# Performance work log

Measured on AMD Instinct MI355X. Metric: run time of the kernel, lower is better.

## Reference

```python
import jax, jax.numpy as jnp
import numpy as np

B, S, H = 32, 64, 512
ATT = 128


def _window_index_tables(seq_len):
    # Enumerate all contiguous windows of size 2..S, same set (order-independent
    # for the softmax-weighted sum) as the torch double loop.
    starts, ends = [], []
    for w in range(2, seq_len + 1):
        for s in range(0, seq_len - w + 1):
            starts.append(s)
            ends.append(s + w)
    starts = np.asarray(starts, np.int32)
    ends = np.asarray(ends, np.int32)
    widths = ends - starts
    ks = np.floor(np.log2(widths)).astype(np.int32)  # sparse-table level per window
    e2 = ends - (1 << ks)                            # second gather position
    return starts, e2, ks


def setup_inputs() -> dict:
    key = jax.random.key(0)
    k0, k1, k2, k3, k4 = jax.random.split(key, 5)
    return {
        "lstm_out": jax.random.normal(k0, (B, S, H), dtype=jnp.float32),
        "W1": jax.random.normal(k1, (H, ATT), dtype=jnp.float32) * 0.05,
        "b1": jax.random.normal(k2, (ATT,), dtype=jnp.float32) * 0.05,
        "W2": jax.random.normal(k3, (ATT, 1), dtype=jnp.float32) * 0.05,
        "b2": jax.random.normal(k4, (1,), dtype=jnp.float32) * 0.05,
    }


def reference(lstm_out, W1, b1, W2, b2):
    b, s, h = lstm_out.shape
    # Sparse table: M[k][:, i] = max over lstm_out[:, i : i+2^k] (clipped to s).
    n_levels = int(np.floor(np.log2(s))) + 1
    tables = [lstm_out]
    for k in range(1, n_levels):
        half = 1 << (k - 1)
        prev = tables[-1]
        shifted = jnp.concatenate(
            [prev[:, half:], jnp.full((b, half, h), -jnp.inf, prev.dtype)], axis=1)
        tables.append(jnp.maximum(prev, shifted))
    Mstack = jnp.stack(tables)  # [K, B, S, H]

    starts, e2, ks = _window_index_tables(s)
    # Range max of each window = max of two overlapping power-of-two blocks.
    pooled = jnp.maximum(Mstack[ks, :, starts], Mstack[ks, :, e2])  # [n_win, B, H]
    pooled = jnp.transpose(pooled, (1, 0, 2))  # [B, n_win, H]

    hid = jax.nn.relu(jnp.einsum("bnh,ha->bna", pooled, W1) + b1)
    scores = jnp.einsum("bna,ao->bno", hid, W2) + b2  # [B, n_win, 1]
    attn = jax.nn.softmax(scores, axis=1)
    return jnp.sum(attn * pooled, axis=1)  # [B, H]
```

## Files before the change

### kernel.cpp

```cpp
#include <hip/hip_runtime.h>
#include <stdint.h>


typedef unsigned short u16;
typedef unsigned int u32;

#define B_    32
#define S_    64
#define H_    512
#define ATT_  128
#define NWIN  2016
#define NLEV  7
#define TLEV  6

typedef __bf16 bf16x8 __attribute__((ext_vector_type(8)));
typedef float  f32x4  __attribute__((ext_vector_type(4)));

__device__ __forceinline__ float asf(u32 i) {
  union { u32 i; float f; } v; v.i = i; return v.f;
}
__device__ __forceinline__ u32 asu(float f) {
  union { float f; u32 i; } v; v.f = f; return v.i;
}
__device__ __forceinline__ float bf2f(u16 u) { return asf(((u32)u) << 16); }
__device__ __forceinline__ u16 f2bf(float f) {
  u32 i = asu(f);
  i += 0x7fffu + ((i >> 16) & 1u);
  return (u16)(i >> 16);
}
__device__ __forceinline__ u32 bfmax2(u32 a, u32 b) {
  float a0 = asf(a << 16), a1 = asf(a & 0xffff0000u);
  float b0 = asf(b << 16), b1 = asf(b & 0xffff0000u);
  u32 m0 = asu(fmaxf(a0, b0)), m1 = asu(fmaxf(a1, b1));
  return (m1 & 0xffff0000u) | (m0 >> 16);
}
__device__ __forceinline__ uint4 bfmax8(uint4 a, uint4 b) {
  uint4 m;
  m.x = bfmax2(a.x, b.x); m.y = bfmax2(a.y, b.y);
  m.z = bfmax2(a.z, b.z); m.w = bfmax2(a.w, b.w);
  return m;
}
__device__ __forceinline__ bf16x8 as_bf16x8(uint4 v) {
  union { uint4 u; bf16x8 h; } c; c.u = v; return c.h;
}

__launch_bounds__(256)
__global__ void k01_init(const float* __restrict__ lstm, const float* __restrict__ W1,
                         u16* __restrict__ table, u16* __restrict__ w1t,
                         u16* __restrict__ widx) {
  int bid = blockIdx.x, tid = threadIdx.x;
  __shared__ u16 bufA[64 * 64], bufB[64 * 64];

  {
    int idx = bid * 256 + tid;
    int n = idx >> 9, kq = idx & 511;
    w1t[idx] = f2bf(W1[kq * ATT_ + n]);
  }
  if (bid < 8) {
    int n = bid * 256 + tid;
    if (n < NWIN) {
      int w = 2, rem = n;
      while (rem >= 65 - w) { rem -= 65 - w; ++w; }
      int s = rem;
      int k = 31 - __clz(w);
      int e2 = s + w - (1 << k);
      widx[n] = (u16)(s | (e2 << 6) | (k << 12));
    }
  }

  int hc = bid & 7, b = bid >> 3;
  const float* src = lstm + (size_t)b * S_ * H_ + hc * 64;
  u16* tb = table + (size_t)b * TLEV * S_ * H_ + hc * 64;
  for (int t = tid; t < 64 * 16; t += 256) {
    int r = t >> 4, c4 = t & 15;
    float4 f = *reinterpret_cast<const float4*>(src + r * H_ + c4 * 4);
    ushort4 u;
    u.x = f2bf(f.x); u.y = f2bf(f.y); u.z = f2bf(f.z); u.w = f2bf(f.w);
    *reinterpret_cast<ushort4*>(&bufA[r * 64 + c4 * 4]) = u;
  }
  u16* pa = bufA; u16* pb = bufB;
  for (int k = 1; k < NLEV; ++k) {
    __syncthreads();
    int half = 1 << (k - 1);
    u16* dst_g = tb + (size_t)(k - 1) * S_ * H_;
    for (int t = tid; t < 64 * 16; t += 256) {
      int r = t >> 4, c4 = t & 15;
      int r2 = r + half; if (r2 > 63) r2 = 63;
      uint2 a  = *reinterpret_cast<const uint2*>(&pa[r  * 64 + c4 * 4]);
      uint2 bq = *reinterpret_cast<const uint2*>(&pa[r2 * 64 + c4 * 4]);
      uint2 m; m.x = bfmax2(a.x, bq.x); m.y = bfmax2(a.y, bq.y);
      *reinterpret_cast<uint2*>(&pb[r * 64 + c4 * 4]) = m;
      *reinterpret_cast<uint2*>(dst_g + r * H_ + c4 * 4) = m;
    }
    u16* tmp = pa; pa = pb; pb = tmp;
  }
}

__launch_bounds__(256, 1)
__global__ void k2_scores(const u16* __restrict__ table, const u16* __restrict__ w1t,
                          const float* __restrict__ b1, const float* __restrict__ w2,
                          const u16* __restrict__ widx, float* __restrict__ scores) {
  const int b = blockIdx.y, mt = blockIdx.x;
  __shared__ u16 Ts[2][128 * 64];
  __shared__ u16 Bs[2][128 * 64];
  __shared__ u16 widx_l[256];
  __shared__ float b1s[128], w2s[128];
  int tid = threadIdx.x;
  {
    int n = mt * 256 + tid; if (n > NWIN - 1) n = NWIN - 1;
    widx_l[tid] = widx[n];
  }
  if (tid < 128) { b1s[tid] = b1[tid]; w2s[tid] = w2[tid]; }
  __syncthreads();

  const int lv_lo = widx_l[0] >> 12;
  const u16* tb = table + (size_t)b * TLEV * S_ * H_ + (size_t)(lv_lo - 1) * S_ * H_;

  const u16* gT[4]; const u16* gB[4]; int sl[4];
#pragma unroll
  for (int p = 0; p < 4; ++p) {
    int slot = p * 256 + tid;
    int r = slot >> 3, c = slot & 7;
    int csw = (c ^ (r & 7)) * 8;
    gT[p] = tb  + r * H_ + csw;
    gB[p] = w1t + r * H_ + csw;
    sl[p] = slot * 8;
  }

#define DMA(KC, BSEL) do {                                                     \
    int ko_ = (KC) * 64;                                                       \
    _Pragma("unroll")                                                          \
    for (int p_ = 0; p_ < 4; ++p_) {                                           \
      __builtin_amdgcn_global_load_lds(                                        \
          (const __attribute__((address_space(1))) void*)(gT[p_] + ko_),       \
          (__attribute__((address_space(3))) void*)(&Ts[(BSEL)][sl[p_]]),      \
          16, 0, 0);                                                           \
      __builtin_amdgcn_global_load_lds(                                        \
          (const __attribute__((address_space(1))) void*)(gB[p_] + ko_),       \
          (__attribute__((address_space(3))) void*)(&Bs[(BSEL)][sl[p_]]),      \
          16, 0, 0);                                                           \
    }                                                                          \
  } while (0)

  int wid = tid >> 6, lane = tid & 63;
  int lrow = lane & 15, quad = lane >> 4;

  int aoff[4][2][2];
#pragma unroll
  for (int mi = 0; mi < 4; ++mi) {
    int pk = widx_l[wid * 64 + mi * 16 + lrow];
    int s = pk & 63, e2 = (pk >> 6) & 63, lv = (pk >> 12) - lv_lo;
    int rs = lv * 64 + s, re = lv * 64 + e2;
#pragma unroll
    for (int k2i = 0; k2i < 2; ++k2i) {
      int c = quad + k2i * 4;
      aoff[mi][k2i][0] = rs * 64 + ((c ^ (rs & 7)) * 8);
      aoff[mi][k2i][1] = re * 64 + ((c ^ (re & 7)) * 8);
    }
  }
  int boff[8][2];
#pragma unroll
  for (int j = 0; j < 8; ++j) {
    int n = j * 16 + lrow;
#pragma unroll
    for (int k2i = 0; k2i < 2; ++k2i) {
      int c = quad + k2i * 4;
      boff[j][k2i] = n * 64 + ((c ^ (n & 7)) * 8);
    }
  }

  f32x4 acc[4][8];
#pragma unroll
  for (int mi = 0; mi < 4; ++mi)
#pragma unroll
    for (int j = 0; j < 8; ++j) acc[mi][j] = (f32x4){0.f, 0.f, 0.f, 0.f};

  DMA(0, 0);

  for (int kc = 0; kc < 8; ++kc) {
    __syncthreads();
    if (kc < 7) DMA(kc + 1, (kc + 1) & 1);
    const u16* Tc = Ts[kc & 1];
    const u16* Bc = Bs[kc & 1];
#pragma unroll
    for (int k2i = 0; k2i < 2; ++k2i) {
      bf16x8 bfr[8];
#pragma unroll
      for (int j = 0; j < 8; ++j)
        bfr[j] = *reinterpret_cast<const bf16x8*>(&Bc[boff[j][k2i]]);
#pragma unroll
      for (int mi = 0; mi < 4; ++mi) {
        uint4 va = *reinterpret_cast<const uint4*>(&Tc[aoff[mi][k2i][0]]);
        uint4 vb = *reinterpret_cast<const uint4*>(&Tc[aoff[mi][k2i][1]]);
        bf16x8 af = as_bf16x8(bfmax8(va, vb));
#pragma unroll
        for (int j = 0; j < 8; ++j)
          acc[mi][j] = __builtin_amdgcn_mfma_f32_16x16x32_bf16(af, bfr[j], acc[mi][j], 0, 0, 0);
      }
    }
  }
#undef DMA

#pragma unroll
  for (int mi = 0; mi < 4; ++mi) {
#pragma unroll
    for (int r = 0; r < 4; ++r) {
      float p = 0.f;
#pragma unroll
      for (int j = 0; j < 8; ++j) {
        int n = j * 16 + lrow;
        float v = acc[mi][j][r] + b1s[n];
        p += (v > 0.f ? v : 0.f) * w2s[n];
      }
      p += __shfl_xor(p, 1, 16);
      p += __shfl_xor(p, 2, 16);
      p += __shfl_xor(p, 4, 16);
      p += __shfl_xor(p, 8, 16);
      if (lrow == 0) {
        int nw = mt * 256 + wid * 64 + mi * 16 + quad * 4 + r;
        if (nw < NWIN) scores[b * NWIN + nw] = p;
      }
    }
  }
}

__launch_bounds__(256)
__global__ void k34_out(const u16* __restrict__ table, const float* __restrict__ scores,
                        const u16* __restrict__ widx, float* __restrict__ out) {
  int hc = blockIdx.x, b = blockIdx.y, tid = threadIdx.x;
  __shared__ u16 Tl[TLEV * 64 * 64];
  __shared__ float attn_l[NWIN];
  __shared__ u16 widx_l[NWIN];
  __shared__ float red[4][64];
  __shared__ float wredM[4], wredS[4];
  const u16* tb = table + (size_t)b * TLEV * S_ * H_;
  int h0 = hc * 64;
  int lane = tid & 63, wid = tid >> 6;

  for (int t = tid; t < TLEV * 64 * 8; t += 256) {
    int row = t >> 3, c = t & 7;
    uint4 v = *reinterpret_cast<const uint4*>(tb + row * H_ + h0 + c * 8);
    *reinterpret_cast<uint4*>(&Tl[row * 64 + ((c ^ (row & 7)) * 8)]) = v;
  }
  for (int n = tid; n < NWIN; n += 256) widx_l[n] = widx[n];

  float mx = -1e30f;
  for (int n = tid; n < NWIN; n += 256) {
    float v = scores[b * NWIN + n];
    attn_l[n] = v;
    mx = fmaxf(mx, v);
  }
#pragma unroll
  for (int off = 32; off > 0; off >>= 1) mx = fmaxf(mx, __shfl_xor(mx, off, 64));
  if (lane == 0) wredM[wid] = mx;
  __syncthreads();
  mx = fmaxf(fmaxf(wredM[0], wredM[1]), fmaxf(wredM[2], wredM[3]));
  float sum = 0.f;
  for (int n = tid; n < NWIN; n += 256) {
    float e = __expf(attn_l[n] - mx);
    attn_l[n] = e;
    sum += e;
  }
#pragma unroll
  for (int off = 32; off > 0; off >>= 1) sum += __shfl_xor(sum, off, 64);
  if (lane == 0) wredS[wid] = sum;
  __syncthreads();
  float inv = 1.f / (wredS[0] + wredS[1] + wredS[2] + wredS[3]);

  int hq = tid & 7, g = tid >> 3;
  float acc[8];
#pragma unroll
  for (int j = 0; j < 8; ++j) acc[j] = 0.f;
  for (int i = 0; i < 63; ++i) {
    int n = g * 63 + i;
    int pk = widx_l[n];
    float a = attn_l[n];
    int s = pk & 63, e2 = (pk >> 6) & 63, lv = pk >> 12;
    int rs = (lv - 1) * 64 + s, re = (lv - 1) * 64 + e2;
    uint4 va = *reinterpret_cast<const uint4*>(&Tl[rs * 64 + ((hq ^ (rs & 7)) * 8)]);
    uint4 vb = *reinterpret_cast<const uint4*>(&Tl[re * 64 + ((hq ^ (re & 7)) * 8)]);
    u32 ua, ub;
#define ACC2(UA, UB, J0) do {                                            \
      float xa0 = asf((UA) << 16), xa1 = asf((UA) & 0xffff0000u);        \
      float xb0 = asf((UB) << 16), xb1 = asf((UB) & 0xffff0000u);        \
      acc[(J0)]     = fmaf(a, fmaxf(xa0, xb0), acc[(J0)]);               \
      acc[(J0) + 1] = fmaf(a, fmaxf(xa1, xb1), acc[(J0) + 1]);           \
    } while (0)
    ua = va.x; ub = vb.x; ACC2(ua, ub, 0);
    ua = va.y; ub = vb.y; ACC2(ua, ub, 2);
    ua = va.z; ub = vb.z; ACC2(ua, ub, 4);
    ua = va.w; ub = vb.w; ACC2(ua, ub, 6);
#undef ACC2
  }

#pragma unroll
  for (int j = 0; j < 8; ++j) {
    acc[j] += __shfl_xor(acc[j], 8, 64);
    acc[j] += __shfl_xor(acc[j], 16, 64);
    acc[j] += __shfl_xor(acc[j], 32, 64);
  }
  if (lane < 8) {
#pragma unroll
    for (int j = 0; j < 8; ++j) red[wid][hq * 8 + j] = acc[j];
  }
  __syncthreads();
  if (tid < 64) {
    float s2 = red[0][tid] + red[1][tid] + red[2][tid] + red[3][tid];
    out[b * H_ + h0 + tid] = s2 * inv;
  }
}

extern "C" void kernel_launch(void* const* d_in, const int* in_sizes, int n_in,
                              void* d_out, int out_size, void* d_ws, size_t ws_size,
                              hipStream_t stream) {
  const float* lstm = (const float*)d_in[0];
  const float* W1   = (const float*)d_in[1];
  const float* b1   = (const float*)d_in[2];
  const float* W2   = (const float*)d_in[3];
  float* out = (float*)d_out;

  char* ws = (char*)d_ws;
  u16*   widx   = (u16*)(ws + 0);
  u16*   w1t    = (u16*)(ws + 4096);
  u16*   table  = (u16*)(ws + 135168);
  float* scores = (float*)(ws + 12718080);

  k01_init <<<256, 256, 0, stream>>>(lstm, W1, table, w1t, widx);
  k2_scores<<<dim3(8, B_), 256, 0, stream>>>(table, w1t, b1, W2, widx, scores);
  k34_out  <<<dim3(8, B_), 256, 0, stream>>>(table, scores, widx, out);
}
```

Before: 116.0 us.

## Fuse three kernels into one cooperative kernel with grid syncs and LDS-resident tables

```diff
diff --git a/kernel.cpp b/kernel.cpp
--- a/kernel.cpp
+++ b/kernel.cpp
@@ -1,6 +1,9 @@
 #include <hip/hip_runtime.h>
+#include <hip/hip_cooperative_groups.h>
 #include <stdint.h>
 
+
+namespace cg = cooperative_groups;
 
 typedef unsigned short u16;
 typedef unsigned int u32;
@@ -44,13 +47,289 @@
   union { uint4 u; bf16x8 h; } c; c.u = v; return c.h;
 }
 
+__launch_bounds__(256, 1)
+__global__ void fused_all(const float* __restrict__ lstm, const float* __restrict__ W1,
+                          const float* __restrict__ b1, const float* __restrict__ w2,
+                          u16* __restrict__ table, u16* __restrict__ w1t,
+                          u16* __restrict__ widx, float* __restrict__ scores,
+                          float* __restrict__ out) {
+  __shared__ __align__(16) u16 Tslab[TLEV * 64 * 64];
+  __shared__ __align__(16) char auxraw[67072];
+  const int bid = blockIdx.x, tid = threadIdx.x;
+  cg::grid_group grid = cg::this_grid();
+
+  {
+    {
+      int idx = bid * 256 + tid;
+      int n = idx >> 9, kq = idx & 511;
+      w1t[idx] = f2bf(W1[kq * ATT_ + n]);
+    }
+    if (bid < 8) {
+      int n = bid * 256 + tid;
+      if (n < NWIN) {
+        int w = 2, rem = n;
+        while (rem >= 65 - w) { rem -= 65 - w; ++w; }
+        int s = rem;
+        int k = 31 - __clz(w);
+        int e2 = s + w - (1 << k);
+        widx[n] = (u16)(s | (e2 << 6) | (k << 12));
+      }
+    }
+
+    int hc = bid & 7, bb = bid >> 3;
+    const float* src = lstm + (size_t)bb * S_ * H_ + hc * 64;
+    u16* tb = table + (size_t)bb * TLEV * S_ * H_ + hc * 64;
+    u16* buf0 = (u16*)auxraw;
+
+    for (int t = tid; t < 64 * 16; t += 256) {
+      int r = t >> 4, c4 = t & 15;
+      float4 f = *reinterpret_cast<const float4*>(src + r * H_ + c4 * 4);
+      ushort4 u;
+      u.x = f2bf(f.x); u.y = f2bf(f.y); u.z = f2bf(f.z); u.w = f2bf(f.w);
+      *reinterpret_cast<ushort4*>(&buf0[r * 64 + c4 * 4]) = u;
+    }
+    __syncthreads();
+
+    for (int k = 1; k < NLEV; ++k) {
+      int half = 1 << (k - 1);
+      u16* dstT = Tslab + (k - 1) * 4096;
+      const u16* srcL = (k == 1) ? buf0 : (Tslab + (k - 2) * 4096);
+      const int swz = (k != 1);
+      u16* dst_g = tb + (size_t)(k - 1) * S_ * H_;
+      for (int t = tid; t < 64 * 8; t += 256) {
+        int r = t >> 3, c = t & 7;
+        int r2 = r + half; if (r2 > 63) r2 = 63;
+        int ca = swz ? (c ^ (r  & 7)) : c;
+        int cb = swz ? (c ^ (r2 & 7)) : c;
+        uint4 a  = *reinterpret_cast<const uint4*>(&srcL[r  * 64 + ca * 8]);
+        uint4 bq = *reinterpret_cast<const uint4*>(&srcL[r2 * 64 + cb * 8]);
+        uint4 m = bfmax8(a, bq);
+        *reinterpret_cast<uint4*>(&dstT[r * 64 + ((c ^ (r & 7)) * 8)]) = m;
+        *reinterpret_cast<uint4*>(dst_g + r * H_ + c * 8) = m;
+      }
+      __syncthreads();
+    }
+  }
+
+  __threadfence();
+  grid.sync();
+  __threadfence();
+
+  {
+    const int bb = bid >> 3, mt = bid & 7;
+    u16* TsB = (u16*)auxraw;
+    u16* BsB = (u16*)(auxraw + 32768);
+    u16* widx_l = (u16*)(auxraw + 65536);
+    float* b1s = (float*)(auxraw + 66048);
+    float* w2s = (float*)(auxraw + 66560);
+
+    {
+      int n = mt * 256 + tid; if (n > NWIN - 1) n = NWIN - 1;
+      widx_l[tid] = widx[n];
+    }
+    if (tid < 128) { b1s[tid] = b1[tid]; w2s[tid] = w2[tid]; }
+    __syncthreads();
+
+    const int lv_lo = widx_l[0] >> 12;
+    const u16* tb = table + (size_t)bb * TLEV * S_ * H_ + (size_t)(lv_lo - 1) * S_ * H_;
+
+    const u16* gT[4]; const u16* gB[4]; int sl[4];
+#pragma unroll
+    for (int p = 0; p < 4; ++p) {
+      int slot = p * 256 + tid;
+      int r = slot >> 3, c = slot & 7;
+      int csw = (c ^ (r & 7)) * 8;
+      gT[p] = tb  + r * H_ + csw;
+      gB[p] = w1t + r * H_ + csw;
+      sl[p] = slot * 8;
+    }
+
+#define DMA(KC, BSEL) do {                                                     \
+    int ko_ = (KC) * 64;                                                       \
+    _Pragma("unroll")                                                          \
+    for (int p_ = 0; p_ < 4; ++p_) {                                           \
+      __builtin_amdgcn_global_load_lds(                                        \
+          (const __attribute__((address_space(1))) void*)(gT[p_] + ko_),       \
+          (__attribute__((address_space(3))) void*)(TsB + (BSEL) * 8192 + sl[p_]), \
+          16, 0, 0);                                                           \
+      __builtin_amdgcn_global_load_lds(                                        \
+          (const __attribute__((address_space(1))) void*)(gB[p_] + ko_),       \
+          (__attribute__((address_space(3))) void*)(BsB + (BSEL) * 8192 + sl[p_]), \
+          16, 0, 0);                                                           \
+    }                                                                          \
+  } while (0)
+
+    int wid = tid >> 6, lane = tid & 63;
+    int lrow = lane & 15, quad = lane >> 4;
+
+    int aoff[4][2][2];
+#pragma unroll
+    for (int mi = 0; mi < 4; ++mi) {
+      int pk = widx_l[wid * 64 + mi * 16 + lrow];
+      int s = pk & 63, e2 = (pk >> 6) & 63, lv = (pk >> 12) - lv_lo;
+      int rs = lv * 64 + s, re = lv * 64 + e2;
+#pragma unroll
+      for (int k2i = 0; k2i < 2; ++k2i) {
+        int c = quad + k2i * 4;
+        aoff[mi][k2i][0] = rs * 64 + ((c ^ (rs & 7)) * 8);
+        aoff[mi][k2i][1] = re * 64 + ((c ^ (re & 7)) * 8);
+      }
+    }
+    int boff[8][2];
+#pragma unroll
+    for (int j = 0; j < 8; ++j) {
+      int n = j * 16 + lrow;
+#pragma unroll
+      for (int k2i = 0; k2i < 2; ++k2i) {
+        int c = quad + k2i * 4;
+        boff[j][k2i] = n * 64 + ((c ^ (n & 7)) * 8);
+      }
+    }
+
+    f32x4 acc[4][8];
+#pragma unroll
+    for (int mi = 0; mi < 4; ++mi)
+#pragma unroll
+      for (int j = 0; j < 8; ++j) acc[mi][j] = (f32x4){0.f, 0.f, 0.f, 0.f};
+
+    DMA(0, 0);
+
+    for (int kc = 0; kc < 8; ++kc) {
+      __syncthreads();
+      if (kc < 7) DMA(kc + 1, (kc + 1) & 1);
+      const u16* Tc = TsB + (kc & 1) * 8192;
+      const u16* Bc = BsB + (kc & 1) * 8192;
+#pragma unroll
+      for (int k2i = 0; k2i < 2; ++k2i) {
+        bf16x8 bfr[8];
+#pragma unroll
+        for (int j = 0; j < 8; ++j)
+          bfr[j] = *reinterpret_cast<const bf16x8*>(&Bc[boff[j][k2i]]);
+#pragma unroll
+        for (int mi = 0; mi < 4; ++mi) {
+          uint4 va = *reinterpret_cast<const uint4*>(&Tc[aoff[mi][k2i][0]]);
+          uint4 vb = *reinterpret_cast<const uint4*>(&Tc[aoff[mi][k2i][1]]);
+          bf16x8 af = as_bf16x8(bfmax8(va, vb));
+#pragma unroll
+          for (int j = 0; j < 8; ++j)
+            acc[mi][j] = __builtin_amdgcn_mfma_f32_16x16x32_bf16(af, bfr[j], acc[mi][j], 0, 0, 0);
+        }
+      }
+    }
+#undef DMA
+
+#pragma unroll
+    for (int mi = 0; mi < 4; ++mi) {
+#pragma unroll
+      for (int r = 0; r < 4; ++r) {
+        float p = 0.f;
+#pragma unroll
+        for (int j = 0; j < 8; ++j) {
+          int n = j * 16 + lrow;
+          float v = acc[mi][j][r] + b1s[n];
+          p += (v > 0.f ? v : 0.f) * w2s[n];
+        }
+        p += __shfl_xor(p, 1, 16);
+        p += __shfl_xor(p, 2, 16);
+        p += __shfl_xor(p, 4, 16);
+        p += __shfl_xor(p, 8, 16);
+        if (lrow == 0) {
+          int nw = mt * 256 + wid * 64 + mi * 16 + quad * 4 + r;
+          if (nw < NWIN) scores[bb * NWIN + nw] = p;
+        }
+      }
+    }
+  }
+
+  __threadfence();
+  grid.sync();
+  __threadfence();
+
+  {
+    const int hc = bid & 7, bb = bid >> 3;
+    float* attn_l = (float*)auxraw;
+    u16*  widxC  = (u16*)(auxraw + 8064);
+    float* red   = (float*)(auxraw + 12096);
+    float* wredM = (float*)(auxraw + 13120);
+    float* wredS = (float*)(auxraw + 13136);
+    int h0 = hc * 64;
+    int lane = tid & 63, wid = tid >> 6;
+
+    for (int n = tid; n < NWIN; n += 256) widxC[n] = widx[n];
+
+    float mx = -1e30f;
+    for (int n = tid; n < NWIN; n += 256) {
+      float v = scores[bb * NWIN + n];
+      attn_l[n] = v;
+      mx = fmaxf(mx, v);
+    }
+#pragma unroll
+    for (int off = 32; off > 0; off >>= 1) mx = fmaxf(mx, __shfl_xor(mx, off, 64));
+    if (lane == 0) wredM[wid] = mx;
+    __syncthreads();
+    mx = fmaxf(fmaxf(wredM[0], wredM[1]), fmaxf(wredM[2], wredM[3]));
+    float sum = 0.f;
+    for (int n = tid; n < NWIN; n += 256) {
+      float e = __expf(attn_l[n] - mx);
+      attn_l[n] = e;
+      sum += e;
+    }
+#pragma unroll
+    for (int off = 32; off > 0; off >>= 1) sum += __shfl_xor(sum, off, 64);
+    if (lane == 0) wredS[wid] = sum;
+    __syncthreads();
+    float inv = 1.f / (wredS[0] + wredS[1] + wredS[2] + wredS[3]);
+
+    int hq = tid & 7, g = tid >> 3;
+    float acc[8];
+#pragma unroll
+    for (int j = 0; j < 8; ++j) acc[j] = 0.f;
+    for (int i = 0; i < 63; ++i) {
+      int n = g * 63 + i;
+      int pk = widxC[n];
+      float a = attn_l[n];
+      int s = pk & 63, e2 = (pk >> 6) & 63, lv = pk >> 12;
+      int rs = (lv - 1) * 64 + s, re = (lv - 1) * 64 + e2;
+      uint4 va = *reinterpret_cast<const uint4*>(&Tslab[rs * 64 + ((hq ^ (rs & 7)) * 8)]);
+      uint4 vb = *reinterpret_cast<const uint4*>(&Tslab[re * 64 + ((hq ^ (re & 7)) * 8)]);
+      u32 ua, ub;
+#define ACC2(UA, UB, J0) do {                                            \
+      float xa0 = asf((UA) << 16), xa1 = asf((UA) & 0xffff0000u);        \
+      float xb0 = asf((UB) << 16), xb1 = asf((UB) & 0xffff0000u);        \
+      acc[(J0)]     = fmaf(a, fmaxf(xa0, xb0), acc[(J0)]);               \
+      acc[(J0) + 1] = fmaf(a, fmaxf(xa1, xb1), acc[(J0) + 1]);           \
+    } while (0)
+      ua = va.x; ub = vb.x; ACC2(ua, ub, 0);
+      ua = va.y; ub = vb.y; ACC2(ua, ub, 2);
+      ua = va.z; ub = vb.z; ACC2(ua, ub, 4);
+      ua = va.w; ub = vb.w; ACC2(ua, ub, 6);
+#undef ACC2
+    }
+
+#pragma unroll
+    for (int j = 0; j < 8; ++j) {
+      acc[j] += __shfl_xor(acc[j], 8, 64);
+      acc[j] += __shfl_xor(acc[j], 16, 64);
+      acc[j] += __shfl_xor(acc[j], 32, 64);
+    }
+    if (lane < 8) {
+#pragma unroll
+      for (int j = 0; j < 8; ++j) red[wid * 64 + hq * 8 + j] = acc[j];
+    }
+    __syncthreads();
+    if (tid < 64) {
+      float s2 = red[0 * 64 + tid] + red[1 * 64 + tid] + red[2 * 64 + tid] + red[3 * 64 + tid];
+      out[bb * H_ + h0 + tid] = s2 * inv;
+    }
+  }
+}
+
 __launch_bounds__(256)
 __global__ void k01_init(const float* __restrict__ lstm, const float* __restrict__ W1,
                          u16* __restrict__ table, u16* __restrict__ w1t,
                          u16* __restrict__ widx) {
   int bid = blockIdx.x, tid = threadIdx.x;
   __shared__ u16 bufA[64 * 64], bufB[64 * 64];
-
   {
     int idx = bid * 256 + tid;
     int n = idx >> 9, kq = idx & 511;
@@ -67,7 +346,6 @@
       widx[n] = (u16)(s | (e2 << 6) | (k << 12));
     }
   }
-
   int hc = bid & 7, b = bid >> 3;
   const float* src = lstm + (size_t)b * S_ * H_ + hc * 64;
   u16* tb = table + (size_t)b * TLEV * S_ * H_ + hc * 64;
@@ -325,7 +603,16 @@
   u16*   table  = (u16*)(ws + 135168);
   float* scores = (float*)(ws + 12718080);
 
-  k01_init <<<256, 256, 0, stream>>>(lstm, W1, table, w1t, widx);
-  k2_scores<<<dim3(8, B_), 256, 0, stream>>>(table, w1t, b1, W2, widx, scores);
-  k34_out  <<<dim3(8, B_), 256, 0, stream>>>(table, scores, widx, out);
-}
+  void* kargs[] = { (void*)&lstm, (void*)&W1, (void*)&b1, (void*)&W2,
+                    (void*)&table, (void*)&w1t, (void*)&widx,
+                    (void*)&scores, (void*)&out };
+  hipError_t st = hipLaunchCooperativeKernel((const void*)fused_all,
+                                             dim3(256), dim3(256),
+                                             kargs, 0, stream);
+  if (st != hipSuccess) {
+    (void)hipGetLastError();
+    k01_init <<<256, 256, 0, stream>>>(lstm, W1, table, w1t, widx);
+    k2_scores<<<dim3(8, B_), 256, 0, stream>>>(table, w1t, b1, W2, widx, scores);
+    k34_out  <<<dim3(8, B_), 256, 0, stream>>>(table, scores, widx, out);
+  }
+}
```

New measurement: 237.9 us. 2.05x slower.
